# Performance work log

Hardware: AMD Instinct MI355X
Metric: run time of the kernel (lower is better)

Reference implementation:

```python
import jax, jax.numpy as jnp
import numpy as np

N_NODES = 50000


def gcn_conv(x, src, dst, deg_inv_sqrt, W, b, n_nodes):
    # GCNConv: h = x @ W; msg = norm * h[src]; out = scatter_add(msg, dst) + b
    h = x @ W  # [N, out]
    norm = deg_inv_sqrt[src] * deg_inv_sqrt[dst]  # symmetric normalization
    msg = h[src] * norm[:, None]  # [E+N, out]
    out = jax.ops.segment_sum(msg, dst, num_segments=n_nodes)
    return out + b


def setup_inputs() -> dict:
    key = jax.random.key(0)
    k_x, k_e, k_w1, k_w2 = jax.random.split(key, 4)
    in_c, hid, out_c = 256, 64, 64
    x = jax.random.normal(k_x, (N_NODES, 256), dtype=jnp.float32)
    edge_index = jax.random.randint(k_e, (2, 1600000), 0, N_NODES, dtype=jnp.int64)
    # Glorot-ish weights, zero bias as in GCNConv defaults
    W1 = jax.random.normal(k_w1, (in_c, hid), dtype=jnp.float32) / np.sqrt(in_c)
    b1 = jnp.zeros((hid,), dtype=jnp.float32)
    W2 = jax.random.normal(k_w2, (hid, out_c), dtype=jnp.float32) / np.sqrt(hid)
    b2 = jnp.zeros((out_c,), dtype=jnp.float32)
    return {"x": x, "edge_index": edge_index, "W1": W1, "b1": b1, "W2": W2, "b2": b2}


def reference(x, edge_index, W1, b1, W2, b2):
    n = x.shape[0]
    loops = jnp.arange(n, dtype=edge_index.dtype)
    src = jnp.concatenate([edge_index[0], loops])  # add self-loops
    dst = jnp.concatenate([edge_index[1], loops])
    deg = jax.ops.segment_sum(jnp.ones_like(dst, dtype=x.dtype), dst, num_segments=n)
    deg_inv_sqrt = jnp.where(deg > 0, jax.lax.rsqrt(deg), 0.0)
    h = gcn_conv(x, src, dst, deg_inv_sqrt, W1, b1, n)
    h = jax.nn.relu(h)
    out = gcn_conv(h, src, dst, deg_inv_sqrt, W2, b2, n)
    return out
```

## Files before the change

### kernel.cpp

```cpp
#include <hip/hip_runtime.h>
#include <hip/hip_bf16.h>


#define NB_MAX 1024

__device__ inline unsigned short f2bf(float f) {
    unsigned u = __builtin_bit_cast(unsigned, f);
    return (unsigned short)((u + 0x7FFFu + ((u >> 16) & 1u)) >> 16);
}
__device__ inline float blo(unsigned u) {
    return __builtin_bit_cast(float, u << 16);
}
__device__ inline float bhi(unsigned u) {
    return __builtin_bit_cast(float, u & 0xFFFF0000u);
}


__global__ __launch_bounds__(1024) void k_hist(const int* __restrict__ ei, int E,
                                               int nb, int chunk,
                                               int* __restrict__ histT) {
    __shared__ int h[NB_MAX];
    for (int i = threadIdx.x; i < nb; i += 1024) h[i] = 0;
    __syncthreads();
    int e0 = blockIdx.x * chunk, e1 = min(E, e0 + chunk);
    for (int e = e0 + threadIdx.x; e < e1; e += 1024)
        atomicAdd(&h[ei[E + e] >> 6], 1);
    __syncthreads();
    for (int b = threadIdx.x; b < nb; b += 1024)
        histT[b * 256 + blockIdx.x] = h[b];
}


__global__ __launch_bounds__(256) void k_scan_cols(int* __restrict__ histT,
                                                   int* __restrict__ total) {
    __shared__ int sm[256];
    int b = blockIdx.x, t = threadIdx.x;
    int v = histT[b * 256 + t];
    sm[t] = v;
    __syncthreads();
    for (int off = 1; off < 256; off <<= 1) {
        int u = (t >= off) ? sm[t - off] : 0;
        __syncthreads();
        sm[t] += u;
        __syncthreads();
    }
    histT[b * 256 + t] = sm[t] - v;
    if (t == 255) total[b] = sm[255];
}


__global__ __launch_bounds__(1024) void k_scan_totals(const int* __restrict__ total,
                                                      int* __restrict__ base, int nb) {
    __shared__ int sm[1024];
    int t = threadIdx.x;
    int v = (t < nb) ? total[t] : 0;
    sm[t] = v;
    __syncthreads();
    for (int off = 1; off < 1024; off <<= 1) {
        int u = (t >= off) ? sm[t - off] : 0;
        __syncthreads();
        sm[t] += u;
        __syncthreads();
    }
    if (t < nb) base[t] = sm[t] - v;
    if (t == nb - 1) base[nb] = sm[t];
}


__global__ __launch_bounds__(1024) void k_scatter(const int* __restrict__ ei, int E,
                                                  int nb, int chunk,
                                                  const int* __restrict__ histT,
                                                  const int* __restrict__ base,
                                                  unsigned* __restrict__ packed) {
    __shared__ int cur[NB_MAX];
    for (int b = threadIdx.x; b < nb; b += 1024)
        cur[b] = base[b] + histT[b * 256 + blockIdx.x];
    __syncthreads();
    int e0 = blockIdx.x * chunk, e1 = min(E, e0 + chunk);
    for (int e = e0 + threadIdx.x; e < e1; e += 1024) {
        int s = ei[e], d = ei[E + e];
        int pos = atomicAdd(&cur[d >> 6], 1);
        packed[pos] = (unsigned)s | ((unsigned)(d & 63) << 16);
    }
}


__global__ __launch_bounds__(1024) void k_csr(const unsigned* __restrict__ packed,
                                              const int* __restrict__ base,
                                              int n,
                                              int* __restrict__ qbeg,
                                              int* __restrict__ qcnt,
                                              float* __restrict__ dinv,
                                              unsigned short* __restrict__ ssrcp,
                                              unsigned short* __restrict__ hs1,
                                              unsigned short* __restrict__ hs2) {
    __shared__ int cnt[64];
    __shared__ int cur[64];
    const int b = blockIdx.x, t = threadIdx.x;
    const int p0 = base[b], p1 = base[b + 1];
    if (t < 64) cnt[t] = 0;
    __syncthreads();
    for (int p = p0 + t; p < p1; p += 1024)
        atomicAdd(&cnt[(packed[p] >> 16) & 63], 1);
    __syncthreads();
    if (t < 64) {
        int deg = cnt[t];
        int pdeg = (deg + 1) & ~1;
        int sum = pdeg;
#pragma unroll
        for (int d = 1; d < 64; d <<= 1) {
            int u = __shfl_up(sum, d, 64);
            if (t >= d) sum += u;
        }
        int excl = sum - pdeg;
        int pb = (2 + p0 + 128 * b + 1) & ~1;
        int start = pb + excl;
        int node = (b << 6) + t;
        if (node < n) {
            qbeg[node] = start >> 1;
            qcnt[node] = pdeg >> 1;
            dinv[node] = 1.0f / sqrtf((float)(deg + 1));
        }
        cur[t] = start;
    }
    __syncthreads();
    for (int p = p0 + t; p < p1; p += 1024) {
        unsigned k = packed[p];
        int pos = atomicAdd(&cur[(k >> 16) & 63], 1);
        ssrcp[pos] = (unsigned short)(k & 0xFFFFu);
    }
    __syncthreads();
    if (t < 64 && (cnt[t] & 1))
        ssrcp[cur[t]] = (unsigned short)n;
    if (b == 0) {
        if (t < 64) {
            hs1[(size_t)n * 64 + t] = 0;
            hs2[(size_t)n * 64 + t] = 0;
        }
        if (t == 0) {
            ssrcp[0] = (unsigned short)n;
            ssrcp[1] = (unsigned short)n;
        }
    }
}


#define FMA4(A, s, wv)                                                         \
    (A).x += (s) * (wv).x; (A).y += (s) * (wv).y;                              \
    (A).z += (s) * (wv).z; (A).w += (s) * (wv).w;

template <int K>
__global__ __launch_bounds__(256) void k_gemm(const float* __restrict__ X,
                                              const float* __restrict__ W,
                                              const float* __restrict__ dinv,
                                              unsigned short* __restrict__ HS,
                                              int n) {
    __shared__ float xl[64][36];
    __shared__ float wl[32][64];

    const int t = threadIdx.x;
    const int tc = t & 15;
    const int tr = t >> 4;
    const int row0 = blockIdx.x * 64;

    float4 acc[4];
    acc[0] = acc[1] = acc[2] = acc[3] = make_float4(0.f, 0.f, 0.f, 0.f);

    for (int k0 = 0; k0 < K; k0 += 32) {
#pragma unroll
        for (int i = 0; i < 2; ++i) {
            int idx = i * 256 + t;
            int r = idx >> 3, f4 = idx & 7;
            int gr = row0 + r;
            float4 v = make_float4(0.f, 0.f, 0.f, 0.f);
            if (gr < n) v = *(const float4*)(X + (size_t)gr * K + k0 + f4 * 4);
            *(float4*)&xl[r][f4 * 4] = v;
        }
#pragma unroll
        for (int i = 0; i < 2; ++i) {
            int idx = i * 256 + t;
            int kr = idx >> 4, f4 = idx & 15;
            *(float4*)&wl[kr][f4 * 4] =
                *(const float4*)(W + (size_t)(k0 + kr) * 64 + f4 * 4);
        }
        __syncthreads();

#pragma unroll
        for (int kk = 0; kk < 32; kk += 4) {
            float4 xv0 = *(float4*)&xl[tr * 4 + 0][kk];
            float4 xv1 = *(float4*)&xl[tr * 4 + 1][kk];
            float4 xv2 = *(float4*)&xl[tr * 4 + 2][kk];
            float4 xv3 = *(float4*)&xl[tr * 4 + 3][kk];
            float4 wv0 = *(float4*)&wl[kk + 0][tc * 4];
            float4 wv1 = *(float4*)&wl[kk + 1][tc * 4];
            float4 wv2 = *(float4*)&wl[kk + 2][tc * 4];
            float4 wv3 = *(float4*)&wl[kk + 3][tc * 4];

            FMA4(acc[0], xv0.x, wv0); FMA4(acc[0], xv0.y, wv1);
            FMA4(acc[0], xv0.z, wv2); FMA4(acc[0], xv0.w, wv3);
            FMA4(acc[1], xv1.x, wv0); FMA4(acc[1], xv1.y, wv1);
            FMA4(acc[1], xv1.z, wv2); FMA4(acc[1], xv1.w, wv3);
            FMA4(acc[2], xv2.x, wv0); FMA4(acc[2], xv2.y, wv1);
            FMA4(acc[2], xv2.z, wv2); FMA4(acc[2], xv2.w, wv3);
            FMA4(acc[3], xv3.x, wv0); FMA4(acc[3], xv3.y, wv1);
            FMA4(acc[3], xv3.z, wv2); FMA4(acc[3], xv3.w, wv3);
        }
        __syncthreads();
    }

#pragma unroll
    for (int ri = 0; ri < 4; ++ri) {
        int gr = row0 + tr * 4 + ri;
        if (gr < n) {
            float dv = dinv[gr];
            float4 o = acc[ri];
            ushort4 pk;
            pk.x = f2bf(o.x * dv); pk.y = f2bf(o.y * dv);
            pk.z = f2bf(o.z * dv); pk.w = f2bf(o.w * dv);
            *(ushort4*)(HS + (size_t)gr * 64 + tc * 4) = pk;
        }
    }
}


template <bool RELU>
__global__ __launch_bounds__(256) void k_agg(const unsigned short* __restrict__ hs,
                      const int* __restrict__ qbeg,
                      const int* __restrict__ qcnt,
                      const unsigned short* __restrict__ ssrcp,
                      const float* __restrict__ dinv,
                      const float* __restrict__ bias,
                      float* __restrict__ out, int n) {
    int node = blockIdx.x * 4 + (threadIdx.x >> 6);
    if (node >= n) return;
    node = __builtin_amdgcn_readfirstlane(node);
    const int lane = threadIdx.x & 63;
    const int c = lane & 7;
    const int shH = (lane & 8) ? 16 : 0;

    const uint4* hs4 = (const uint4*)hs;
    const unsigned* ssu = (const unsigned*)ssrcp;

    const int q0 = qbeg[node];
    const int m  = qcnt[node];

    const uint4 sv = hs4[node * 8 + c];
    const float dv = dinv[node];
    const float4 bv0 = *(const float4*)(bias + 8 * c);
    const float4 bv1 = *(const float4*)(bias + 8 * c + 4);

    float ax[8];
#pragma unroll
    for (int k = 0; k < 8; ++k) ax[k] = 0.f;

    int qb = 0;
    for (; qb + 8 <= m; qb += 8) {
        unsigned ssl[8];
#pragma unroll
        for (int j = 0; j < 8; ++j) ssl[j] = ssu[q0 + qb + j];
        uint4 v[2];
#pragma unroll
        for (int i = 0; i < 2; ++i) {
            unsigned w = (lane & 32) ? ((lane & 16) ? ssl[4 * i + 3] : ssl[4 * i + 2])
                                     : ((lane & 16) ? ssl[4 * i + 1] : ssl[4 * i + 0]);
            int s = (int)((w >> shH) & 0xFFFFu);
            v[i] = hs4[s * 8 + c];
        }
#pragma unroll
        for (int i = 0; i < 2; ++i) {
            ax[0] += blo(v[i].x); ax[1] += bhi(v[i].x);
            ax[2] += blo(v[i].y); ax[3] += bhi(v[i].y);
            ax[4] += blo(v[i].z); ax[5] += bhi(v[i].z);
            ax[6] += blo(v[i].w); ax[7] += bhi(v[i].w);
        }
    }
    const int rem = m - qb;
    if (rem) {
        unsigned ssl[8];
#pragma unroll
        for (int j = 0; j < 8; ++j) {
            int q = (j < rem) ? (q0 + qb + j) : 0;
            ssl[j] = ssu[q];
        }
        uint4 v[2];
#pragma unroll
        for (int i = 0; i < 2; ++i) {
            unsigned w = (lane & 32) ? ((lane & 16) ? ssl[4 * i + 3] : ssl[4 * i + 2])
                                     : ((lane & 16) ? ssl[4 * i + 1] : ssl[4 * i + 0]);
            int s = (int)((w >> shH) & 0xFFFFu);
            v[i] = hs4[s * 8 + c];
        }
#pragma unroll
        for (int i = 0; i < 2; ++i) {
            ax[0] += blo(v[i].x); ax[1] += bhi(v[i].x);
            ax[2] += blo(v[i].y); ax[3] += bhi(v[i].y);
            ax[4] += blo(v[i].z); ax[5] += bhi(v[i].z);
            ax[6] += blo(v[i].w); ax[7] += bhi(v[i].w);
        }
    }

#pragma unroll
    for (int k = 0; k < 8; ++k) {
        ax[k] += __shfl_xor(ax[k], 8, 64);
        ax[k] += __shfl_xor(ax[k], 16, 64);
        ax[k] += __shfl_xor(ax[k], 32, 64);
    }

    float r[8];
    r[0] = dv * (ax[0] + blo(sv.x)) + bv0.x;
    r[1] = dv * (ax[1] + bhi(sv.x)) + bv0.y;
    r[2] = dv * (ax[2] + blo(sv.y)) + bv0.z;
    r[3] = dv * (ax[3] + bhi(sv.y)) + bv0.w;
    r[4] = dv * (ax[4] + blo(sv.z)) + bv1.x;
    r[5] = dv * (ax[5] + bhi(sv.z)) + bv1.y;
    r[6] = dv * (ax[6] + blo(sv.w)) + bv1.z;
    r[7] = dv * (ax[7] + bhi(sv.w)) + bv1.w;
    if (RELU) {
#pragma unroll
        for (int k = 0; k < 8; ++k) r[k] = fmaxf(r[k], 0.f);
    }
    if (lane < 16) {
        float4 o = (lane & 8) ? make_float4(r[4], r[5], r[6], r[7])
                              : make_float4(r[0], r[1], r[2], r[3]);
        *(float4*)(out + (size_t)node * 64 + 8 * c + 4 * ((lane >> 3) & 1)) = o;
    }
}


extern "C" void kernel_launch(void* const* d_in, const int* in_sizes, int n_in,
                              void* d_out, int out_size, void* d_ws, size_t ws_size,
                              hipStream_t stream) {
    const float* x  = (const float*)d_in[0];
    const int*   ei = (const int*)d_in[1];
    const float* W1 = (const float*)d_in[2];
    const float* b1 = (const float*)d_in[3];
    const float* W2 = (const float*)d_in[4];
    const float* b2 = (const float*)d_in[5];

    const int n = in_sizes[0] / 256;
    const int E = in_sizes[1] / 2;
    const int nb = (n + 63) >> 6;
    const int chunk = (E + 255) / 256;

    char* ws = (char*)d_ws;
    auto carve = [&](size_t bytes) {
        void* p = (void*)ws;
        ws += (bytes + 255) & ~(size_t)255;
        return p;
    };
    int*            histT  = (int*)carve((size_t)nb * 256 * 4);
    int*            total  = (int*)carve((size_t)nb * 4);
    int*            base   = (int*)carve((size_t)(nb + 1) * 4);
    unsigned*       packed = (unsigned*)carve((size_t)E * 4);
    unsigned short* ssrcp  = (unsigned short*)carve(((size_t)E + 128 * nb + 256) * 2);
    int*            qbeg   = (int*)carve((size_t)n * 4);
    int*            qcnt   = (int*)carve((size_t)n * 4);
    float*          dinv   = (float*)carve((size_t)n * 4);
    unsigned short* hs1    = (unsigned short*)carve((size_t)(n + 1) * 64 * 2);
    float*          hB     = (float*)carve((size_t)n * 64 * 4);
    unsigned short* hs2    = (unsigned short*)carve((size_t)(n + 1) * 64 * 2);

    k_hist<<<256, 1024, 0, stream>>>(ei, E, nb, chunk, histT);
    k_scan_cols<<<nb, 256, 0, stream>>>(histT, total);
    k_scan_totals<<<1, 1024, 0, stream>>>(total, base, nb);
    k_scatter<<<256, 1024, 0, stream>>>(ei, E, nb, chunk, histT, base, packed);
    k_csr<<<nb, 1024, 0, stream>>>(packed, base, n, qbeg, qcnt, dinv, ssrcp,
                                   hs1, hs2);

    const int nbG = (n + 63) / 64;

    k_gemm<256><<<nbG, 256, 0, stream>>>(x, W1, dinv, hs1, n);
    k_agg<true><<<(n + 3) / 4, 256, 0, stream>>>(hs1, qbeg, qcnt, ssrcp, dinv,
                                                 b1, hB, n);

    k_gemm<64><<<nbG, 256, 0, stream>>>(hB, W2, dinv, hs2, n);
    k_agg<false><<<(n + 3) / 4, 256, 0, stream>>>(hs2, qbeg, qcnt, ssrcp, dinv,
                                                  b2, (float*)d_out, n);
}
```

Baseline: 215.6 us.

## Split bf16 feature table into two 32-channel planes, aggregate each plane separately

The GEMM now writes the scaled bf16 features as two column planes of 32 channels, each (n+1)x32, instead of one 64-wide row table. Each aggregation is launched twice, once per plane, with a 4-lane-per-neighbor gather that handles 16 neighbors per wave iteration. The goal is to shrink the gathered table per pass (about 3.2MB) so it stays cache-resident and random gathers hit L2. The cost is re-reading the CSR indices twice and twice the launches. Output stores also become nontemporal.

```diff
diff --git a/kernel.cpp b/kernel.cpp
--- a/kernel.cpp
+++ b/kernel.cpp
@@ -3,6 +3,8 @@
 
 
 #define NB_MAX 1024
+
+typedef float vfloat4 __attribute__((ext_vector_type(4)));
 
 __device__ inline unsigned short f2bf(float f) {
     unsigned u = __builtin_bit_cast(unsigned, f);
@@ -134,8 +136,9 @@
         ssrcp[cur[t]] = (unsigned short)n;
     if (b == 0) {
         if (t < 64) {
-            hs1[(size_t)n * 64 + t] = 0;
-            hs2[(size_t)n * 64 + t] = 0;
+            int p = t >> 5, col = t & 31;
+            hs1[((size_t)p * (n + 1) + n) * 32 + col] = 0;
+            hs2[((size_t)p * (n + 1) + n) * 32 + col] = 0;
         }
         if (t == 0) {
             ssrcp[0] = (unsigned short)n;
@@ -208,6 +211,8 @@
         __syncthreads();
     }
 
+    const int pl = tc >> 3;
+    const int pc = (tc & 7) * 4;
 #pragma unroll
     for (int ri = 0; ri < 4; ++ri) {
         int gr = row0 + tr * 4 + ri;
@@ -217,37 +222,40 @@
             ushort4 pk;
             pk.x = f2bf(o.x * dv); pk.y = f2bf(o.y * dv);
             pk.z = f2bf(o.z * dv); pk.w = f2bf(o.w * dv);
-            *(ushort4*)(HS + (size_t)gr * 64 + tc * 4) = pk;
+            *(ushort4*)(HS + ((size_t)pl * (n + 1) + gr) * 32 + pc) = pk;
         }
     }
 }
 
 
 template <bool RELU>
-__global__ __launch_bounds__(256) void k_agg(const unsigned short* __restrict__ hs,
+__global__ __launch_bounds__(256) void k_agg(
+                      const unsigned short* __restrict__ hs,
                       const int* __restrict__ qbeg,
                       const int* __restrict__ qcnt,
                       const unsigned short* __restrict__ ssrcp,
                       const float* __restrict__ dinv,
                       const float* __restrict__ bias,
-                      float* __restrict__ out, int n) {
+                      float* __restrict__ out, int n, int plane) {
     int node = blockIdx.x * 4 + (threadIdx.x >> 6);
     if (node >= n) return;
     node = __builtin_amdgcn_readfirstlane(node);
     const int lane = threadIdx.x & 63;
-    const int c = lane & 7;
-    const int shH = (lane & 8) ? 16 : 0;
-
-    const uint4* hs4 = (const uint4*)hs;
+    const int c = lane & 3;
+    const int g = lane >> 2;
+    const int shH = (g & 1) ? 16 : 0;
+
+    const uint4* hs4 = (const uint4*)hs + (size_t)plane * (n + 1) * 4;
     const unsigned* ssu = (const unsigned*)ssrcp;
 
     const int q0 = qbeg[node];
     const int m  = qcnt[node];
 
-    const uint4 sv = hs4[node * 8 + c];
+    const uint4 sv = hs4[node * 4 + c];
     const float dv = dinv[node];
-    const float4 bv0 = *(const float4*)(bias + 8 * c);
-    const float4 bv1 = *(const float4*)(bias + 8 * c + 4);
+    const int chb = plane * 32 + 8 * c;
+    const float4 bv0 = *(const float4*)(bias + chb);
+    const float4 bv1 = *(const float4*)(bias + chb + 4);
 
     float ax[8];
 #pragma unroll
@@ -258,21 +266,19 @@
         unsigned ssl[8];
 #pragma unroll
         for (int j = 0; j < 8; ++j) ssl[j] = ssu[q0 + qb + j];
-        uint4 v[2];
-#pragma unroll
-        for (int i = 0; i < 2; ++i) {
-            unsigned w = (lane & 32) ? ((lane & 16) ? ssl[4 * i + 3] : ssl[4 * i + 2])
-                                     : ((lane & 16) ? ssl[4 * i + 1] : ssl[4 * i + 0]);
-            int s = (int)((w >> shH) & 0xFFFFu);
-            v[i] = hs4[s * 8 + c];
-        }
-#pragma unroll
-        for (int i = 0; i < 2; ++i) {
-            ax[0] += blo(v[i].x); ax[1] += bhi(v[i].x);
-            ax[2] += blo(v[i].y); ax[3] += bhi(v[i].y);
-            ax[4] += blo(v[i].z); ax[5] += bhi(v[i].z);
-            ax[6] += blo(v[i].w); ax[7] += bhi(v[i].w);
-        }
+        unsigned a0 = (lane & 8) ? ssl[1] : ssl[0];
+        unsigned a1 = (lane & 8) ? ssl[3] : ssl[2];
+        unsigned a2 = (lane & 8) ? ssl[5] : ssl[4];
+        unsigned a3 = (lane & 8) ? ssl[7] : ssl[6];
+        unsigned b0 = (lane & 16) ? a1 : a0;
+        unsigned b1 = (lane & 16) ? a3 : a2;
+        unsigned w  = (lane & 32) ? b1 : b0;
+        int s = (int)((w >> shH) & 0xFFFFu);
+        uint4 v = hs4[s * 4 + c];
+        ax[0] += blo(v.x); ax[1] += bhi(v.x);
+        ax[2] += blo(v.y); ax[3] += bhi(v.y);
+        ax[4] += blo(v.z); ax[5] += bhi(v.z);
+        ax[6] += blo(v.w); ax[7] += bhi(v.w);
     }
     const int rem = m - qb;
     if (rem) {
@@ -282,25 +288,24 @@
             int q = (j < rem) ? (q0 + qb + j) : 0;
             ssl[j] = ssu[q];
         }
-        uint4 v[2];
-#pragma unroll
-        for (int i = 0; i < 2; ++i) {
-            unsigned w = (lane & 32) ? ((lane & 16) ? ssl[4 * i + 3] : ssl[4 * i + 2])
-                                     : ((lane & 16) ? ssl[4 * i + 1] : ssl[4 * i + 0]);
-            int s = (int)((w >> shH) & 0xFFFFu);
-            v[i] = hs4[s * 8 + c];
-        }
-#pragma unroll
-        for (int i = 0; i < 2; ++i) {
-            ax[0] += blo(v[i].x); ax[1] += bhi(v[i].x);
-            ax[2] += blo(v[i].y); ax[3] += bhi(v[i].y);
-            ax[4] += blo(v[i].z); ax[5] += bhi(v[i].z);
-            ax[6] += blo(v[i].w); ax[7] += bhi(v[i].w);
-        }
+        unsigned a0 = (lane & 8) ? ssl[1] : ssl[0];
+        unsigned a1 = (lane & 8) ? ssl[3] : ssl[2];
+        unsigned a2 = (lane & 8) ? ssl[5] : ssl[4];
+        unsigned a3 = (lane & 8) ? ssl[7] : ssl[6];
+        unsigned b0 = (lane & 16) ? a1 : a0;
+        unsigned b1 = (lane & 16) ? a3 : a2;
+        unsigned w  = (lane & 32) ? b1 : b0;
+        int s = (int)((w >> shH) & 0xFFFFu);
+        uint4 v = hs4[s * 4 + c];
+        ax[0] += blo(v.x); ax[1] += bhi(v.x);
+        ax[2] += blo(v.y); ax[3] += bhi(v.y);
+        ax[4] += blo(v.z); ax[5] += bhi(v.z);
+        ax[6] += blo(v.w); ax[7] += bhi(v.w);
     }
 
 #pragma unroll
     for (int k = 0; k < 8; ++k) {
+        ax[k] += __shfl_xor(ax[k], 4, 64);
         ax[k] += __shfl_xor(ax[k], 8, 64);
         ax[k] += __shfl_xor(ax[k], 16, 64);
         ax[k] += __shfl_xor(ax[k], 32, 64);
@@ -319,10 +324,12 @@
 #pragma unroll
         for (int k = 0; k < 8; ++k) r[k] = fmaxf(r[k], 0.f);
     }
-    if (lane < 16) {
-        float4 o = (lane & 8) ? make_float4(r[4], r[5], r[6], r[7])
-                              : make_float4(r[0], r[1], r[2], r[3]);
-        *(float4*)(out + (size_t)node * 64 + 8 * c + 4 * ((lane >> 3) & 1)) = o;
+    if (lane < 4) {
+        float* po = out + (size_t)node * 64 + chb;
+        vfloat4 o0 = {r[0], r[1], r[2], r[3]};
+        vfloat4 o1 = {r[4], r[5], r[6], r[7]};
+        __builtin_nontemporal_store(o0, (vfloat4*)po);
+        __builtin_nontemporal_store(o1, (vfloat4*)(po + 4));
     }
 }
 
@@ -368,12 +375,17 @@
                                    hs1, hs2);
 
     const int nbG = (n + 63) / 64;
+    const int nbA = (n + 3) / 4;
 
     k_gemm<256><<<nbG, 256, 0, stream>>>(x, W1, dinv, hs1, n);
-    k_agg<true><<<(n + 3) / 4, 256, 0, stream>>>(hs1, qbeg, qcnt, ssrcp, dinv,
-                                                 b1, hB, n);
+    k_agg<true><<<nbA, 256, 0, stream>>>(hs1, qbeg, qcnt, ssrcp, dinv,
+                                         b1, hB, n, 0);
+    k_agg<true><<<nbA, 256, 0, stream>>>(hs1, qbeg, qcnt, ssrcp, dinv,
+                                         b1, hB, n, 1);
 
     k_gemm<64><<<nbG, 256, 0, stream>>>(hB, W2, dinv, hs2, n);
-    k_agg<false><<<(n + 3) / 4, 256, 0, stream>>>(hs2, qbeg, qcnt, ssrcp, dinv,
-                                                  b2, (float*)d_out, n);
-}
+    k_agg<false><<<nbA, 256, 0, stream>>>(hs2, qbeg, qcnt, ssrcp, dinv,
+                                          b2, (float*)d_out, n, 0);
+    k_agg<false><<<nbA, 256, 0, stream>>>(hs2, qbeg, qcnt, ssrcp, dinv,
+                                          b2, (float*)d_out, n, 1);
+}
```

Result: slower. 252.4 us (+17.1%).

## Fuse all GCN stages into one cooperative persistent kernel with grid syncs

Applied to the files above, without the earlier changes.

Replaces the nine separate kernel launches with a single cooperative kernel that loops over virtual blocks per stage and separates stages with grid-wide syncs. The intent is to remove per-launch overhead and tail gaps between dependent stages. It also re-partitions the histogram/scatter into 1024 virtual blocks of 256 threads, with a scan that handles four elements per thread. The persistent grid is capped at occupancy times CU count, so the heavy gather and GEMM stages run with far fewer resident blocks than before and depend on the grid-stride loops to cover the work. Shared memory for all stages is allocated at once, which may reduce occupancy. A non-cooperative fallback path keeps the multi-launch version.

```diff
diff --git a/kernel.cpp b/kernel.cpp
--- a/kernel.cpp
+++ b/kernel.cpp
@@ -1,8 +1,21 @@
 #include <hip/hip_runtime.h>
 #include <hip/hip_bf16.h>
+#include <hip/hip_cooperative_groups.h>
+
+namespace cg = cooperative_groups;
 
 
 #define NB_MAX 1024
+#define NVB    1024
+
+struct GcnP {
+    const float* x; const int* ei; const float* W1; const float* b1;
+    const float* W2; const float* b2;
+    int n, E, nb, chunk;
+    int* histT; int* total; int* base; unsigned* packed;
+    unsigned short* ssrcp; int* qbeg; int* qcnt; float* dinv;
+    unsigned short* hs1; float* hB; unsigned short* hs2; float* out;
+};
 
 __device__ inline unsigned short f2bf(float f) {
     unsigned u = __builtin_bit_cast(unsigned, f);
@@ -16,27 +29,34 @@
 }
 
 
-__global__ __launch_bounds__(1024) void k_hist(const int* __restrict__ ei, int E,
-                                               int nb, int chunk,
-                                               int* __restrict__ histT) {
-    __shared__ int h[NB_MAX];
-    for (int i = threadIdx.x; i < nb; i += 1024) h[i] = 0;
-    __syncthreads();
-    int e0 = blockIdx.x * chunk, e1 = min(E, e0 + chunk);
-    for (int e = e0 + threadIdx.x; e < e1; e += 1024)
+__device__ inline void hist_body(const int* __restrict__ ei, int E, int nb,
+                                 int chunk, int* __restrict__ histT, int vb,
+                                 int* h) {
+    const int t = threadIdx.x;
+    for (int i = t; i < nb; i += 256) h[i] = 0;
+    __syncthreads();
+    int e0 = vb * chunk, e1 = min(E, e0 + chunk);
+    for (int e = e0 + t; e < e1; e += 256)
         atomicAdd(&h[ei[E + e] >> 6], 1);
     __syncthreads();
-    for (int b = threadIdx.x; b < nb; b += 1024)
-        histT[b * 256 + blockIdx.x] = h[b];
-}
-
-
-__global__ __launch_bounds__(256) void k_scan_cols(int* __restrict__ histT,
-                                                   int* __restrict__ total) {
-    __shared__ int sm[256];
-    int b = blockIdx.x, t = threadIdx.x;
-    int v = histT[b * 256 + t];
-    sm[t] = v;
+    for (int b = t; b < nb; b += 256)
+        histT[(size_t)b * NVB + vb] = h[b];
+    __syncthreads();
+}
+
+
+__device__ inline void scan_block(const int* __restrict__ src,
+                                  int* __restrict__ dst, int m,
+                                  int* grand_out, bool write_end, int* sm) {
+    const int t = threadIdx.x;
+    const int idx = t * 4;
+    int a[4]; int s = 0;
+#pragma unroll
+    for (int i = 0; i < 4; ++i) {
+        a[i] = (idx + i < m) ? src[idx + i] : 0;
+        s += a[i];
+    }
+    sm[t] = s;
     __syncthreads();
     for (int off = 1; off < 256; off <<= 1) {
         int u = (t >= off) ? sm[t - off] : 0;
@@ -44,63 +64,53 @@
         sm[t] += u;
         __syncthreads();
     }
-    histT[b * 256 + t] = sm[t] - v;
-    if (t == 255) total[b] = sm[255];
-}
-
-
-__global__ __launch_bounds__(1024) void k_scan_totals(const int* __restrict__ total,
-                                                      int* __restrict__ base, int nb) {
-    __shared__ int sm[1024];
-    int t = threadIdx.x;
-    int v = (t < nb) ? total[t] : 0;
-    sm[t] = v;
-    __syncthreads();
-    for (int off = 1; off < 1024; off <<= 1) {
-        int u = (t >= off) ? sm[t - off] : 0;
-        __syncthreads();
-        sm[t] += u;
-        __syncthreads();
-    }
-    if (t < nb) base[t] = sm[t] - v;
-    if (t == nb - 1) base[nb] = sm[t];
-}
-
-
-__global__ __launch_bounds__(1024) void k_scatter(const int* __restrict__ ei, int E,
-                                                  int nb, int chunk,
-                                                  const int* __restrict__ histT,
-                                                  const int* __restrict__ base,
-                                                  unsigned* __restrict__ packed) {
-    __shared__ int cur[NB_MAX];
-    for (int b = threadIdx.x; b < nb; b += 1024)
-        cur[b] = base[b] + histT[b * 256 + blockIdx.x];
-    __syncthreads();
-    int e0 = blockIdx.x * chunk, e1 = min(E, e0 + chunk);
-    for (int e = e0 + threadIdx.x; e < e1; e += 1024) {
+    int run = sm[t] - s;
+    int grand = sm[255];
+#pragma unroll
+    for (int i = 0; i < 4; ++i) {
+        if (idx + i < m) dst[idx + i] = run;
+        run += a[i];
+    }
+    if (t == 0) {
+        if (grand_out) *grand_out = grand;
+        if (write_end) dst[m] = grand;
+    }
+    __syncthreads();
+}
+
+
+__device__ inline void scatter_body(const int* __restrict__ ei, int E, int nb,
+                                    int chunk, const int* __restrict__ histT,
+                                    const int* __restrict__ base,
+                                    unsigned* __restrict__ packed, int vb,
+                                    int* h) {
+    const int t = threadIdx.x;
+    for (int b = t; b < nb; b += 256)
+        h[b] = base[b] + histT[(size_t)b * NVB + vb];
+    __syncthreads();
+    int e0 = vb * chunk, e1 = min(E, e0 + chunk);
+    for (int e = e0 + t; e < e1; e += 256) {
         int s = ei[e], d = ei[E + e];
-        int pos = atomicAdd(&cur[d >> 6], 1);
+        int pos = atomicAdd(&h[d >> 6], 1);
         packed[pos] = (unsigned)s | ((unsigned)(d & 63) << 16);
     }
-}
-
-
-__global__ __launch_bounds__(1024) void k_csr(const unsigned* __restrict__ packed,
-                                              const int* __restrict__ base,
-                                              int n,
-                                              int* __restrict__ qbeg,
-                                              int* __restrict__ qcnt,
-                                              float* __restrict__ dinv,
-                                              unsigned short* __restrict__ ssrcp,
-                                              unsigned short* __restrict__ hs1,
-                                              unsigned short* __restrict__ hs2) {
-    __shared__ int cnt[64];
-    __shared__ int cur[64];
-    const int b = blockIdx.x, t = threadIdx.x;
+    __syncthreads();
+}
+
+
+__device__ inline void csr_body(const unsigned* __restrict__ packed,
+                                const int* __restrict__ base, int n, int b,
+                                int* __restrict__ qbeg, int* __restrict__ qcnt,
+                                float* __restrict__ dinv,
+                                unsigned short* __restrict__ ssrcp,
+                                unsigned short* __restrict__ hs1,
+                                unsigned short* __restrict__ hs2,
+                                int* cnt, int* cur) {
+    const int t = threadIdx.x;
     const int p0 = base[b], p1 = base[b + 1];
     if (t < 64) cnt[t] = 0;
     __syncthreads();
-    for (int p = p0 + t; p < p1; p += 1024)
+    for (int p = p0 + t; p < p1; p += 256)
         atomicAdd(&cnt[(packed[p] >> 16) & 63], 1);
     __syncthreads();
     if (t < 64) {
@@ -124,7 +134,7 @@
         cur[t] = start;
     }
     __syncthreads();
-    for (int p = p0 + t; p < p1; p += 1024) {
+    for (int p = p0 + t; p < p1; p += 256) {
         unsigned k = packed[p];
         int pos = atomicAdd(&cur[(k >> 16) & 63], 1);
         ssrcp[pos] = (unsigned short)(k & 0xFFFFu);
@@ -142,6 +152,7 @@
             ssrcp[1] = (unsigned short)n;
         }
     }
+    __syncthreads();
 }
 
 
@@ -150,18 +161,14 @@
     (A).z += (s) * (wv).z; (A).w += (s) * (wv).w;
 
 template <int K>
-__global__ __launch_bounds__(256) void k_gemm(const float* __restrict__ X,
-                                              const float* __restrict__ W,
-                                              const float* __restrict__ dinv,
-                                              unsigned short* __restrict__ HS,
-                                              int n) {
-    __shared__ float xl[64][36];
-    __shared__ float wl[32][64];
-
+__device__ inline void gemm_body(const float* __restrict__ X,
+                                 const float* __restrict__ W,
+                                 const float* __restrict__ dinv,
+                                 unsigned short* __restrict__ HS, int n,
+                                 int row0, float (*xl)[36], float (*wl)[64]) {
     const int t = threadIdx.x;
     const int tc = t & 15;
     const int tr = t >> 4;
-    const int row0 = blockIdx.x * 64;
 
     float4 acc[4];
     acc[0] = acc[1] = acc[2] = acc[3] = make_float4(0.f, 0.f, 0.f, 0.f);
@@ -223,15 +230,15 @@
 }
 
 
-template <bool RELU>
-__global__ __launch_bounds__(256) void k_agg(const unsigned short* __restrict__ hs,
-                      const int* __restrict__ qbeg,
-                      const int* __restrict__ qcnt,
-                      const unsigned short* __restrict__ ssrcp,
-                      const float* __restrict__ dinv,
-                      const float* __restrict__ bias,
-                      float* __restrict__ out, int n) {
-    int node = blockIdx.x * 4 + (threadIdx.x >> 6);
+__device__ inline void agg_body(const unsigned short* __restrict__ hs,
+                                const int* __restrict__ qbeg,
+                                const int* __restrict__ qcnt,
+                                const unsigned short* __restrict__ ssrcp,
+                                const float* __restrict__ dinv,
+                                const float* __restrict__ bias,
+                                float* __restrict__ out, int n, int vb,
+                                bool relu) {
+    int node = vb * 4 + ((int)threadIdx.x >> 6);
     if (node >= n) return;
     node = __builtin_amdgcn_readfirstlane(node);
     const int lane = threadIdx.x & 63;
@@ -244,7 +251,7 @@
     const int q0 = qbeg[node];
     const int m  = qcnt[node];
 
-    const uint4 sv = hs4[node * 8 + c];
+    const uint4 sv = hs4[(size_t)node * 8 + c];
     const float dv = dinv[node];
     const float4 bv0 = *(const float4*)(bias + 8 * c);
     const float4 bv1 = *(const float4*)(bias + 8 * c + 4);
@@ -264,7 +271,7 @@
             unsigned w = (lane & 32) ? ((lane & 16) ? ssl[4 * i + 3] : ssl[4 * i + 2])
                                      : ((lane & 16) ? ssl[4 * i + 1] : ssl[4 * i + 0]);
             int s = (int)((w >> shH) & 0xFFFFu);
-            v[i] = hs4[s * 8 + c];
+            v[i] = hs4[(size_t)s * 8 + c];
         }
 #pragma unroll
         for (int i = 0; i < 2; ++i) {
@@ -288,7 +295,7 @@
             unsigned w = (lane & 32) ? ((lane & 16) ? ssl[4 * i + 3] : ssl[4 * i + 2])
                                      : ((lane & 16) ? ssl[4 * i + 1] : ssl[4 * i + 0]);
             int s = (int)((w >> shH) & 0xFFFFu);
-            v[i] = hs4[s * 8 + c];
+            v[i] = hs4[(size_t)s * 8 + c];
         }
 #pragma unroll
         for (int i = 0; i < 2; ++i) {
@@ -315,7 +322,7 @@
     r[5] = dv * (ax[5] + bhi(sv.z)) + bv1.y;
     r[6] = dv * (ax[6] + blo(sv.w)) + bv1.z;
     r[7] = dv * (ax[7] + bhi(sv.w)) + bv1.w;
-    if (RELU) {
+    if (relu) {
 #pragma unroll
         for (int k = 0; k < 8; ++k) r[k] = fmaxf(r[k], 0.f);
     }
@@ -327,20 +334,121 @@
 }
 
 
+__global__ __launch_bounds__(256, 4) void k_fused(GcnP P) {
+    __shared__ int   h[NB_MAX];
+    __shared__ int   sm[256];
+    __shared__ int   cnt[64], cur[64];
+    __shared__ float xl[64][36];
+    __shared__ float wl[32][64];
+
+    cg::grid_group grid = cg::this_grid();
+    const int bx = blockIdx.x, gsz = gridDim.x;
+
+    for (int vb = bx; vb < NVB; vb += gsz)
+        hist_body(P.ei, P.E, P.nb, P.chunk, P.histT, vb, h);
+    grid.sync();
+
+    for (int b = bx; b < P.nb; b += gsz)
+        scan_block(P.histT + (size_t)b * NVB, P.histT + (size_t)b * NVB,
+                   NVB, &P.total[b], false, sm);
+    grid.sync();
+
+    if (bx == 0) scan_block(P.total, P.base, P.nb, nullptr, true, sm);
+    grid.sync();
+
+    for (int vb = bx; vb < NVB; vb += gsz)
+        scatter_body(P.ei, P.E, P.nb, P.chunk, P.histT, P.base, P.packed, vb,
+                     h);
+    grid.sync();
+
+    for (int b = bx; b < P.nb; b += gsz)
+        csr_body(P.packed, P.base, P.n, b, P.qbeg, P.qcnt, P.dinv, P.ssrcp,
+                 P.hs1, P.hs2, cnt, cur);
+    grid.sync();
+
+    const int nbG = (P.n + 63) >> 6;
+    const int nbA = (P.n + 3) >> 2;
+
+    for (int vb = bx; vb < nbG; vb += gsz)
+        gemm_body<256>(P.x, P.W1, P.dinv, P.hs1, P.n, vb << 6, xl, wl);
+    grid.sync();
+
+    for (int vb = bx; vb < nbA; vb += gsz)
+        agg_body(P.hs1, P.qbeg, P.qcnt, P.ssrcp, P.dinv, P.b1, P.hB, P.n, vb,
+                 true);
+    grid.sync();
+
+    for (int vb = bx; vb < nbG; vb += gsz)
+        gemm_body<64>(P.hB, P.W2, P.dinv, P.hs2, P.n, vb << 6, xl, wl);
+    grid.sync();
+
+    for (int vb = bx; vb < nbA; vb += gsz)
+        agg_body(P.hs2, P.qbeg, P.qcnt, P.ssrcp, P.dinv, P.b2, P.out, P.n, vb,
+                 false);
+}
+
+
+__global__ __launch_bounds__(256) void c_hist(GcnP P) {
+    __shared__ int h[NB_MAX];
+    for (int vb = blockIdx.x; vb < NVB; vb += gridDim.x)
+        hist_body(P.ei, P.E, P.nb, P.chunk, P.histT, vb, h);
+}
+__global__ __launch_bounds__(256) void c_scan_cols(GcnP P) {
+    __shared__ int sm[256];
+    int b = blockIdx.x;
+    scan_block(P.histT + (size_t)b * NVB, P.histT + (size_t)b * NVB, NVB,
+               &P.total[b], false, sm);
+}
+__global__ __launch_bounds__(256) void c_scan_tot(GcnP P) {
+    __shared__ int sm[256];
+    scan_block(P.total, P.base, P.nb, nullptr, true, sm);
+}
+__global__ __launch_bounds__(256) void c_scatter(GcnP P) {
+    __shared__ int h[NB_MAX];
+    for (int vb = blockIdx.x; vb < NVB; vb += gridDim.x)
+        scatter_body(P.ei, P.E, P.nb, P.chunk, P.histT, P.base, P.packed, vb,
+                     h);
+}
+__global__ __launch_bounds__(256) void c_csr(GcnP P) {
+    __shared__ int cnt[64], cur[64];
+    csr_body(P.packed, P.base, P.n, blockIdx.x, P.qbeg, P.qcnt, P.dinv,
+             P.ssrcp, P.hs1, P.hs2, cnt, cur);
+}
+__global__ __launch_bounds__(256) void c_gemm1(GcnP P) {
+    __shared__ float xl[64][36];
+    __shared__ float wl[32][64];
+    gemm_body<256>(P.x, P.W1, P.dinv, P.hs1, P.n, blockIdx.x << 6, xl, wl);
+}
+__global__ __launch_bounds__(256) void c_agg1(GcnP P) {
+    agg_body(P.hs1, P.qbeg, P.qcnt, P.ssrcp, P.dinv, P.b1, P.hB, P.n,
+             blockIdx.x, true);
+}
+__global__ __launch_bounds__(256) void c_gemm2(GcnP P) {
+    __shared__ float xl[64][36];
+    __shared__ float wl[32][64];
+    gemm_body<64>(P.hB, P.W2, P.dinv, P.hs2, P.n, blockIdx.x << 6, xl, wl);
+}
+__global__ __launch_bounds__(256) void c_agg2(GcnP P) {
+    agg_body(P.hs2, P.qbeg, P.qcnt, P.ssrcp, P.dinv, P.b2, P.out, P.n,
+             blockIdx.x, false);
+}
+
+
 extern "C" void kernel_launch(void* const* d_in, const int* in_sizes, int n_in,
                               void* d_out, int out_size, void* d_ws, size_t ws_size,
                               hipStream_t stream) {
-    const float* x  = (const float*)d_in[0];
-    const int*   ei = (const int*)d_in[1];
-    const float* W1 = (const float*)d_in[2];
-    const float* b1 = (const float*)d_in[3];
-    const float* W2 = (const float*)d_in[4];
-    const float* b2 = (const float*)d_in[5];
-
-    const int n = in_sizes[0] / 256;
-    const int E = in_sizes[1] / 2;
-    const int nb = (n + 63) >> 6;
-    const int chunk = (E + 255) / 256;
+    GcnP P;
+    P.x  = (const float*)d_in[0];
+    P.ei = (const int*)d_in[1];
+    P.W1 = (const float*)d_in[2];
+    P.b1 = (const float*)d_in[3];
+    P.W2 = (const float*)d_in[4];
+    P.b2 = (const float*)d_in[5];
+
+    P.n = in_sizes[0] / 256;
+    P.E = in_sizes[1] / 2;
+    P.nb = (P.n + 63) >> 6;
+    P.chunk = (P.E + NVB - 1) / NVB;
 
     char* ws = (char*)d_ws;
     auto carve = [&](size_t bytes) {
@@ -348,32 +456,52 @@
         ws += (bytes + 255) & ~(size_t)255;
         return p;
     };
-    int*            histT  = (int*)carve((size_t)nb * 256 * 4);
-    int*            total  = (int*)carve((size_t)nb * 4);
-    int*            base   = (int*)carve((size_t)(nb + 1) * 4);
-    unsigned*       packed = (unsigned*)carve((size_t)E * 4);
-    unsigned short* ssrcp  = (unsigned short*)carve(((size_t)E + 128 * nb + 256) * 2);
-    int*            qbeg   = (int*)carve((size_t)n * 4);
-    int*            qcnt   = (int*)carve((size_t)n * 4);
-    float*          dinv   = (float*)carve((size_t)n * 4);
-    unsigned short* hs1    = (unsigned short*)carve((size_t)(n + 1) * 64 * 2);
-    float*          hB     = (float*)carve((size_t)n * 64 * 4);
-    unsigned short* hs2    = (unsigned short*)carve((size_t)(n + 1) * 64 * 2);
-
-    k_hist<<<256, 1024, 0, stream>>>(ei, E, nb, chunk, histT);
-    k_scan_cols<<<nb, 256, 0, stream>>>(histT, total);
-    k_scan_totals<<<1, 1024, 0, stream>>>(total, base, nb);
-    k_scatter<<<256, 1024, 0, stream>>>(ei, E, nb, chunk, histT, base, packed);
-    k_csr<<<nb, 1024, 0, stream>>>(packed, base, n, qbeg, qcnt, dinv, ssrcp,
-                                   hs1, hs2);
-
-    const int nbG = (n + 63) / 64;
-
-    k_gemm<256><<<nbG, 256, 0, stream>>>(x, W1, dinv, hs1, n);
-    k_agg<true><<<(n + 3) / 4, 256, 0, stream>>>(hs1, qbeg, qcnt, ssrcp, dinv,
-                                                 b1, hB, n);
-
-    k_gemm<64><<<nbG, 256, 0, stream>>>(hB, W2, dinv, hs2, n);
-    k_agg<false><<<(n + 3) / 4, 256, 0, stream>>>(hs2, qbeg, qcnt, ssrcp, dinv,
-                                                  b2, (float*)d_out, n);
-}
+    P.histT  = (int*)carve((size_t)P.nb * NVB * 4);
+    P.total  = (int*)carve((size_t)P.nb * 4);
+    P.base   = (int*)carve((size_t)(P.nb + 1) * 4);
+    P.packed = (unsigned*)carve((size_t)P.E * 4);
+    P.ssrcp  = (unsigned short*)carve(((size_t)P.E + 128 * P.nb + 256) * 2);
+    P.qbeg   = (int*)carve((size_t)P.n * 4);
+    P.qcnt   = (int*)carve((size_t)P.n * 4);
+    P.dinv   = (float*)carve((size_t)P.n * 4);
+    P.hs1    = (unsigned short*)carve((size_t)(P.n + 1) * 64 * 2);
+    P.hB     = (float*)carve((size_t)P.n * 64 * 4);
+    P.hs2    = (unsigned short*)carve((size_t)(P.n + 1) * 64 * 2);
+    P.out    = (float*)d_out;
+
+    static int coop_grid = -2;
+    if (coop_grid == -2) {
+        int maxb = 0, ncu = 0;
+        hipError_t e1 = hipOccupancyMaxActiveBlocksPerMultiprocessor(
+            &maxb, (const void*)k_fused, 256, 0);
+        hipDeviceProp_t prop;
+        hipError_t e2 = hipGetDeviceProperties(&prop, 0);
+        ncu = prop.multiProcessorCount;
+        if (e1 == hipSuccess && e2 == hipSuccess && maxb >= 1 && ncu >= 1) {
+            long g = (long)maxb * ncu;
+            coop_grid = (int)(g < NVB ? g : NVB);
+        } else {
+            coop_grid = 0;
+        }
+    }
+
+    if (coop_grid > 0) {
+        void* args[] = { &P };
+        hipError_t err = hipLaunchCooperativeKernel(
+            (void*)k_fused, dim3(coop_grid), dim3(256), args, 0, stream);
+        if (err == hipSuccess) return;
+        coop_grid = 0;
+    }
+
+    const int nbG = (P.n + 63) >> 6;
+    const int nbA = (P.n + 3) >> 2;
+    c_hist<<<NVB, 256, 0, stream>>>(P);
+    c_scan_cols<<<P.nb, 256, 0, stream>>>(P);
+    c_scan_tot<<<1, 256, 0, stream>>>(P);
+    c_scatter<<<NVB, 256, 0, stream>>>(P);
+    c_csr<<<P.nb, 256, 0, stream>>>(P);
+    c_gemm1<<<nbG, 256, 0, stream>>>(P);
+    c_agg1<<<nbA, 256, 0, stream>>>(P);
+    c_gemm2<<<nbG, 256, 0, stream>>>(P);
+    c_agg2<<<nbA, 256, 0, stream>>>(P);
+}
```

After: 744.2 us. 245% more time.

## Build CSR with global atomics and single-block scan instead of bucketed sort

Applied to the files above, without the earlier changes.

Replaces the histogram/scan/scatter/bucket-CSR pipeline with a per-node degree count via global atomics, a single-block exclusive scan that writes row offsets and normalization, and a direct atomic fill of source indices. This removes the intermediate packed array and two kernel launches. In exchange it relies on scattered global atomics and a serial-ish one-block scan over all nodes. It also widens gather index arithmetic to size_t.

```diff
diff --git a/kernel.cpp b/kernel.cpp
--- a/kernel.cpp
+++ b/kernel.cpp
@@ -1,8 +1,6 @@
 #include <hip/hip_runtime.h>
 #include <hip/hip_bf16.h>
 
-
-#define NB_MAX 1024
 
 __device__ inline unsigned short f2bf(float f) {
     unsigned u = __builtin_bit_cast(unsigned, f);
@@ -16,131 +14,80 @@
 }
 
 
-__global__ __launch_bounds__(1024) void k_hist(const int* __restrict__ ei, int E,
-                                               int nb, int chunk,
-                                               int* __restrict__ histT) {
-    __shared__ int h[NB_MAX];
-    for (int i = threadIdx.x; i < nb; i += 1024) h[i] = 0;
-    __syncthreads();
+__global__ __launch_bounds__(1024) void k_deg(const int* __restrict__ ei, int E,
+                                              int chunk, int* __restrict__ deg) {
     int e0 = blockIdx.x * chunk, e1 = min(E, e0 + chunk);
     for (int e = e0 + threadIdx.x; e < e1; e += 1024)
-        atomicAdd(&h[ei[E + e] >> 6], 1);
+        atomicAdd(&deg[ei[E + e]], 1);
+}
+
+
+__global__ __launch_bounds__(1024) void k_scan(const int* __restrict__ deg, int n,
+                                               int* __restrict__ qbeg,
+                                               int* __restrict__ qcnt,
+                                               float* __restrict__ dinv,
+                                               int* __restrict__ cur,
+                                               unsigned short* __restrict__ ssrcp,
+                                               unsigned short* __restrict__ hs1,
+                                               unsigned short* __restrict__ hs2) {
+    __shared__ int wsum[16];
+    const int t = threadIdx.x;
+    const int per = (n + 1023) >> 10;
+    const int i0 = t * per, i1 = min(n, i0 + per);
+
+    int s = 0;
+    for (int i = i0; i < i1; ++i) s += (deg[i] + 1) & ~1;
+
+    const int lane = t & 63, w = t >> 6;
+    int ps = s;
+#pragma unroll
+    for (int d = 1; d < 64; d <<= 1) {
+        int u = __shfl_up(ps, d, 64);
+        if (lane >= d) ps += u;
+    }
+    if (lane == 63) wsum[w] = ps;
     __syncthreads();
-    for (int b = threadIdx.x; b < nb; b += 1024)
-        histT[b * 256 + blockIdx.x] = h[b];
-}
-
-
-__global__ __launch_bounds__(256) void k_scan_cols(int* __restrict__ histT,
-                                                   int* __restrict__ total) {
-    __shared__ int sm[256];
-    int b = blockIdx.x, t = threadIdx.x;
-    int v = histT[b * 256 + t];
-    sm[t] = v;
+    if (t < 16) {
+        int v = wsum[t];
+#pragma unroll
+        for (int d = 1; d < 16; d <<= 1) {
+            int u = __shfl_up(v, d, 16);
+            if (t >= d) v += u;
+        }
+        wsum[t] = v;
+    }
     __syncthreads();
-    for (int off = 1; off < 256; off <<= 1) {
-        int u = (t >= off) ? sm[t - off] : 0;
-        __syncthreads();
-        sm[t] += u;
-        __syncthreads();
-    }
-    histT[b * 256 + t] = sm[t] - v;
-    if (t == 255) total[b] = sm[255];
-}
-
-
-__global__ __launch_bounds__(1024) void k_scan_totals(const int* __restrict__ total,
-                                                      int* __restrict__ base, int nb) {
-    __shared__ int sm[1024];
-    int t = threadIdx.x;
-    int v = (t < nb) ? total[t] : 0;
-    sm[t] = v;
-    __syncthreads();
-    for (int off = 1; off < 1024; off <<= 1) {
-        int u = (t >= off) ? sm[t - off] : 0;
-        __syncthreads();
-        sm[t] += u;
-        __syncthreads();
-    }
-    if (t < nb) base[t] = sm[t] - v;
-    if (t == nb - 1) base[nb] = sm[t];
-}
-
-
-__global__ __launch_bounds__(1024) void k_scatter(const int* __restrict__ ei, int E,
-                                                  int nb, int chunk,
-                                                  const int* __restrict__ histT,
-                                                  const int* __restrict__ base,
-                                                  unsigned* __restrict__ packed) {
-    __shared__ int cur[NB_MAX];
-    for (int b = threadIdx.x; b < nb; b += 1024)
-        cur[b] = base[b] + histT[b * 256 + blockIdx.x];
-    __syncthreads();
+
+    int base = 2 + (w ? wsum[w - 1] : 0) + (ps - s);
+    for (int i = i0; i < i1; ++i) {
+        int dg = deg[i];
+        int pd = (dg + 1) & ~1;
+        qbeg[i] = base >> 1;
+        qcnt[i] = pd >> 1;
+        dinv[i] = 1.0f / sqrtf((float)(dg + 1));
+        cur[i]  = base;
+        if (dg & 1) ssrcp[base + dg] = (unsigned short)n;
+        base += pd;
+    }
+    if (t < 64) {
+        hs1[(size_t)n * 64 + t] = 0;
+        hs2[(size_t)n * 64 + t] = 0;
+    }
+    if (t == 0) {
+        ssrcp[0] = (unsigned short)n;
+        ssrcp[1] = (unsigned short)n;
+    }
+}
+
+
+__global__ __launch_bounds__(1024) void k_fill(const int* __restrict__ ei, int E,
+                                               int chunk, int* __restrict__ cur,
+                                               unsigned short* __restrict__ ssrcp) {
     int e0 = blockIdx.x * chunk, e1 = min(E, e0 + chunk);
     for (int e = e0 + threadIdx.x; e < e1; e += 1024) {
         int s = ei[e], d = ei[E + e];
-        int pos = atomicAdd(&cur[d >> 6], 1);
-        packed[pos] = (unsigned)s | ((unsigned)(d & 63) << 16);
-    }
-}
-
-
-__global__ __launch_bounds__(1024) void k_csr(const unsigned* __restrict__ packed,
-                                              const int* __restrict__ base,
-                                              int n,
-                                              int* __restrict__ qbeg,
-                                              int* __restrict__ qcnt,
-                                              float* __restrict__ dinv,
-                                              unsigned short* __restrict__ ssrcp,
-                                              unsigned short* __restrict__ hs1,
-                                              unsigned short* __restrict__ hs2) {
-    __shared__ int cnt[64];
-    __shared__ int cur[64];
-    const int b = blockIdx.x, t = threadIdx.x;
-    const int p0 = base[b], p1 = base[b + 1];
-    if (t < 64) cnt[t] = 0;
-    __syncthreads();
-    for (int p = p0 + t; p < p1; p += 1024)
-        atomicAdd(&cnt[(packed[p] >> 16) & 63], 1);
-    __syncthreads();
-    if (t < 64) {
-        int deg = cnt[t];
-        int pdeg = (deg + 1) & ~1;
-        int sum = pdeg;
-#pragma unroll
-        for (int d = 1; d < 64; d <<= 1) {
-            int u = __shfl_up(sum, d, 64);
-            if (t >= d) sum += u;
-        }
-        int excl = sum - pdeg;
-        int pb = (2 + p0 + 128 * b + 1) & ~1;
-        int start = pb + excl;
-        int node = (b << 6) + t;
-        if (node < n) {
-            qbeg[node] = start >> 1;
-            qcnt[node] = pdeg >> 1;
-            dinv[node] = 1.0f / sqrtf((float)(deg + 1));
-        }
-        cur[t] = start;
-    }
-    __syncthreads();
-    for (int p = p0 + t; p < p1; p += 1024) {
-        unsigned k = packed[p];
-        int pos = atomicAdd(&cur[(k >> 16) & 63], 1);
-        ssrcp[pos] = (unsigned short)(k & 0xFFFFu);
-    }
-    __syncthreads();
-    if (t < 64 && (cnt[t] & 1))
-        ssrcp[cur[t]] = (unsigned short)n;
-    if (b == 0) {
-        if (t < 64) {
-            hs1[(size_t)n * 64 + t] = 0;
-            hs2[(size_t)n * 64 + t] = 0;
-        }
-        if (t == 0) {
-            ssrcp[0] = (unsigned short)n;
-            ssrcp[1] = (unsigned short)n;
-        }
+        int pos = atomicAdd(&cur[d], 1);
+        ssrcp[pos] = (unsigned short)s;
     }
 }
 
@@ -244,7 +191,7 @@
     const int q0 = qbeg[node];
     const int m  = qcnt[node];
 
-    const uint4 sv = hs4[node * 8 + c];
+    const uint4 sv = hs4[(size_t)node * 8 + c];
     const float dv = dinv[node];
     const float4 bv0 = *(const float4*)(bias + 8 * c);
     const float4 bv1 = *(const float4*)(bias + 8 * c + 4);
@@ -264,7 +211,7 @@
             unsigned w = (lane & 32) ? ((lane & 16) ? ssl[4 * i + 3] : ssl[4 * i + 2])
                                      : ((lane & 16) ? ssl[4 * i + 1] : ssl[4 * i + 0]);
             int s = (int)((w >> shH) & 0xFFFFu);
-            v[i] = hs4[s * 8 + c];
+            v[i] = hs4[(size_t)s * 8 + c];
         }
 #pragma unroll
         for (int i = 0; i < 2; ++i) {
@@ -288,7 +235,7 @@
             unsigned w = (lane & 32) ? ((lane & 16) ? ssl[4 * i + 3] : ssl[4 * i + 2])
                                      : ((lane & 16) ? ssl[4 * i + 1] : ssl[4 * i + 0]);
             int s = (int)((w >> shH) & 0xFFFFu);
-            v[i] = hs4[s * 8 + c];
+            v[i] = hs4[(size_t)s * 8 + c];
         }
 #pragma unroll
         for (int i = 0; i < 2; ++i) {
@@ -339,7 +286,6 @@
 
     const int n = in_sizes[0] / 256;
     const int E = in_sizes[1] / 2;
-    const int nb = (n + 63) >> 6;
     const int chunk = (E + 255) / 256;
 
     char* ws = (char*)d_ws;
@@ -348,32 +294,30 @@
         ws += (bytes + 255) & ~(size_t)255;
         return p;
     };
-    int*            histT  = (int*)carve((size_t)nb * 256 * 4);
-    int*            total  = (int*)carve((size_t)nb * 4);
-    int*            base   = (int*)carve((size_t)(nb + 1) * 4);
-    unsigned*       packed = (unsigned*)carve((size_t)E * 4);
-    unsigned short* ssrcp  = (unsigned short*)carve(((size_t)E + 128 * nb + 256) * 2);
+    int*            deg    = (int*)carve((size_t)n * 4);
+    int*            cur    = (int*)carve((size_t)n * 4);
     int*            qbeg   = (int*)carve((size_t)n * 4);
     int*            qcnt   = (int*)carve((size_t)n * 4);
     float*          dinv   = (float*)carve((size_t)n * 4);
+    unsigned short* ssrcp  = (unsigned short*)carve(((size_t)E + n + 256) * 2);
     unsigned short* hs1    = (unsigned short*)carve((size_t)(n + 1) * 64 * 2);
     float*          hB     = (float*)carve((size_t)n * 64 * 4);
     unsigned short* hs2    = (unsigned short*)carve((size_t)(n + 1) * 64 * 2);
 
-    k_hist<<<256, 1024, 0, stream>>>(ei, E, nb, chunk, histT);
-    k_scan_cols<<<nb, 256, 0, stream>>>(histT, total);
-    k_scan_totals<<<1, 1024, 0, stream>>>(total, base, nb);
-    k_scatter<<<256, 1024, 0, stream>>>(ei, E, nb, chunk, histT, base, packed);
-    k_csr<<<nb, 1024, 0, stream>>>(packed, base, n, qbeg, qcnt, dinv, ssrcp,
+    hipMemsetAsync(deg, 0, (size_t)n * 4, stream);
+    k_deg<<<256, 1024, 0, stream>>>(ei, E, chunk, deg);
+    k_scan<<<1, 1024, 0, stream>>>(deg, n, qbeg, qcnt, dinv, cur, ssrcp,
                                    hs1, hs2);
+    k_fill<<<256, 1024, 0, stream>>>(ei, E, chunk, cur, ssrcp);
 
     const int nbG = (n + 63) / 64;
+    const int nbA = (n + 3) / 4;
 
     k_gemm<256><<<nbG, 256, 0, stream>>>(x, W1, dinv, hs1, n);
-    k_agg<true><<<(n + 3) / 4, 256, 0, stream>>>(hs1, qbeg, qcnt, ssrcp, dinv,
-                                                 b1, hB, n);
+    k_agg<true><<<nbA, 256, 0, stream>>>(hs1, qbeg, qcnt, ssrcp, dinv,
+                                         b1, hB, n);
 
     k_gemm<64><<<nbG, 256, 0, stream>>>(hB, W2, dinv, hs2, n);
-    k_agg<false><<<(n + 3) / 4, 256, 0, stream>>>(hs2, qbeg, qcnt, ssrcp, dinv,
-                                                  b2, (float*)d_out, n);
-}
+    k_agg<false><<<nbA, 256, 0, stream>>>(hs2, qbeg, qcnt, ssrcp, dinv,
+                                          b2, (float*)d_out, n);
+}
```

Measured after the change: 525.8 us. +143.8%, slower.
